# Kernel optimization log

Measured on AMD Instinct MI355X. Metric: run time of the kernel, lower is better.

The kernel has to match this reference:

```python
import jax, jax.numpy as jnp
import numpy as np

N, E, D, L = 100000, 400000, 300, 5
BN_EPS = 1e-5


def setup_inputs() -> dict:
    key = jax.random.key(0)
    ks = jax.random.split(key, 8)
    x = jax.random.randint(ks[0], (N, 7), 0, 5)
    edge_index = jax.random.randint(ks[1], (2, E), 0, N)
    edge_attr = jax.random.randint(ks[2], (E, 4), 0, 2)
    s = 0.1
    atom_tables = jax.random.normal(ks[3], (7, 119, D), jnp.float32) * s
    bond_tables = jax.random.normal(ks[4], (L, 4, 6, D), jnp.float32) * s
    mlp_w1 = jax.random.normal(ks[5], (L, D, 2 * D), jnp.float32) * (1.0 / np.sqrt(D))
    mlp_b1 = jnp.zeros((L, 2 * D), jnp.float32)
    mlp_w2 = jax.random.normal(ks[6], (L, 2 * D, D), jnp.float32) * (1.0 / np.sqrt(2 * D))
    mlp_b2 = jnp.zeros((L, D), jnp.float32)
    bn_gamma = jnp.ones((L, D), jnp.float32)
    bn_beta = jnp.zeros((L, D), jnp.float32)
    return dict(x=x, edge_index=edge_index, edge_attr=edge_attr,
                atom_tables=atom_tables, bond_tables=bond_tables,
                mlp_w1=mlp_w1, mlp_b1=mlp_b1, mlp_w2=mlp_w2, mlp_b2=mlp_b2,
                bn_gamma=bn_gamma, bn_beta=bn_beta)


def reference(x, edge_index, edge_attr, atom_tables, bond_tables,
              mlp_w1, mlp_b1, mlp_w2, mlp_b2, bn_gamma, bn_beta):
    n = x.shape[0]
    # add self loops (PyG add_self_loops appends them)
    loop = jnp.arange(n)
    src = jnp.concatenate([edge_index[0], loop])  # message source j
    dst = jnp.concatenate([edge_index[1], loop])  # aggregation target i
    self_loop_attr = jnp.zeros((n, 4), edge_attr.dtype).at[:, 0].set(4)
    ea = jnp.concatenate([edge_attr, self_loop_attr], axis=0)  # [E+N, 4]

    # AtomEncoder: sum of 7 per-feature embeddings -> [N, D]
    h = atom_tables[jnp.arange(7), x].sum(axis=1)

    for l in range(L):
        # BondEncoder: sum of 4 per-feature embeddings -> [E+N, D]
        e_emb = bond_tables[l][jnp.arange(4), ea].sum(axis=1)
        # GIN message = x_j + edge_emb, aggr='add' by target node
        msg = h[src] + e_emb
        agg = jax.ops.segment_sum(msg, dst, num_segments=n)
        # GIN update MLP: Linear -> ReLU -> Linear
        hid = jax.nn.relu(agg @ mlp_w1[l] + mlp_b1[l])
        out = hid @ mlp_w2[l] + mlp_b2[l]
        # BatchNorm1d (training mode: batch stats, biased var)
        mu = out.mean(axis=0)
        var = out.var(axis=0)
        out = (out - mu) / jnp.sqrt(var + BN_EPS) * bn_gamma[l] + bn_beta[l]
        # drop_ratio = 0.0 -> dropout is identity; ReLU except last layer
        if l < L - 1:
            out = jax.nn.relu(out)
        h = out
    return h  # JK='last'
```

## Files before the change

### kernel.cpp

```cpp
#include <hip/hip_runtime.h>

typedef unsigned short u16;
typedef unsigned int   u32;
typedef __bf16 bf16x8 __attribute__((ext_vector_type(8)));
typedef float  f32x4  __attribute__((ext_vector_type(4)));

__device__ __forceinline__ u16 f2bf(float f) {
    u32 u = __builtin_bit_cast(u32, f);
    u = u + 0x7fffu + ((u >> 16) & 1u);
    return (u16)(u >> 16);
}
__device__ __forceinline__ float bflo(u32 u) { return __builtin_bit_cast(float, u << 16); }
__device__ __forceinline__ float bfhi(u32 u) { return __builtin_bit_cast(float, u & 0xffff0000u); }
__device__ __forceinline__ u32 pack2(float x, float y) { return (u32)f2bf(x) | ((u32)f2bf(y) << 16); }

__device__ __forceinline__ void gll16(const u16* g, u16* l) {
    __builtin_amdgcn_global_load_lds(
        (const __attribute__((address_space(1))) void*)g,
        (__attribute__((address_space(3))) void*)l, 16, 0, 0);
}

#define NN 100000
#define EE 400000
#define DP 320
#define HP 640

__global__ void count_deg(const int* __restrict__ ei, int* __restrict__ deg, int E) {
    int e = blockIdx.x * 256 + threadIdx.x;
    if (e < E) atomicAdd(&deg[ei[E + e]], 1);
}

__global__ void scan1(const int* __restrict__ deg, int* __restrict__ out, int* __restrict__ bsums, int n) {
    __shared__ int lds[1024];
    int t = threadIdx.x;
    int i = blockIdx.x * 1024 + t;
    int v = (i < n) ? deg[i] : 0;
    lds[t] = v;
    __syncthreads();
    for (int d = 1; d < 1024; d <<= 1) {
        int add = (t >= d) ? lds[t - d] : 0;
        __syncthreads();
        lds[t] += add;
        __syncthreads();
    }
    if (i < n) out[i] = lds[t] - v;
    if (t == 1023) bsums[blockIdx.x] = lds[t];
}

__global__ void scan2(int* __restrict__ bsums, int nb) {
    __shared__ int lds[128];
    int t = threadIdx.x;
    int v = (t < nb) ? bsums[t] : 0;
    lds[t] = v;
    __syncthreads();
    for (int d = 1; d < 128; d <<= 1) {
        int add = (t >= d) ? lds[t - d] : 0;
        __syncthreads();
        lds[t] += add;
        __syncthreads();
    }
    if (t < nb) bsums[t] = lds[t] - v;
}

__global__ void scan3(int* __restrict__ out, const int* __restrict__ bsums, int n, int etot) {
    int i = blockIdx.x * 1024 + threadIdx.x;
    if (i < n) out[i] += bsums[blockIdx.x];
    else if (i == n) out[i] = etot;
}

__global__ void fill_csr(const int* __restrict__ ei, const int* __restrict__ ea,
                         int* __restrict__ cursors, u32* __restrict__ vals, int E) {
    int e = blockIdx.x * 256 + threadIdx.x;
    if (e >= E) return;
    int dst = ei[E + e];
    int src = ei[e];
    u32 code = (u32)((ea[e*4] & 1) | ((ea[e*4+1] & 1) << 1) | ((ea[e*4+2] & 1) << 2) | ((ea[e*4+3] & 1) << 3));
    int pos = atomicAdd(&cursors[dst], 1);
    vals[pos] = ((u32)src << 4) | code;
}

__global__ void conv_w1(const float* __restrict__ w, u16* __restrict__ wt) {
    int id = blockIdx.x * 256 + threadIdx.x;
    if (id >= 5 * HP * DP) return;
    int l = id / (HP * DP);
    int rem = id - l * (HP * DP);
    int n = rem / DP;
    int kidx = rem - n * DP;
    int u = kidx >> 3, e = kidx & 7;
    int kk = ((u ^ (n & 7)) << 3) | e;
    u16 v = 0;
    if (n < 600 && kk < 300) v = f2bf(w[((size_t)l * 300 + kk) * 600 + n]);
    wt[id] = v;
}
__global__ void conv_w2(const float* __restrict__ w, u16* __restrict__ wt) {
    int id = blockIdx.x * 256 + threadIdx.x;
    if (id >= 5 * DP * HP) return;
    int l = id / (DP * HP);
    int rem = id - l * (DP * HP);
    int n = rem / HP;
    int kp = rem - n * HP;
    int up = kp >> 3, e = kp & 7;
    int ul = (up & ~3) | ((up & 3) ^ ((n >> 1) & 3));
    int kk = (ul << 3) | e;
    u16 v = 0;
    if (n < 300 && kk < 600) v = f2bf(w[((size_t)l * 600 + kk) * 300 + n]);
    wt[id] = v;
}

__global__ void atom_enc(const int* __restrict__ x, const float* __restrict__ at, u16* __restrict__ y) {
    const int i = blockIdx.x;
    const int d = threadIdx.x;
    __shared__ int xi[7];
    if (d < 7) xi[d] = x[i * 7 + d];
    __syncthreads();
    u16 v = 0;
    if (d < 300) {
        float s = 0.f;
        #pragma unroll
        for (int f = 0; f < 7; ++f) s += at[(f * 119 + xi[f]) * 300 + d];
        v = f2bf(s);
    }
    y[(size_t)i * DP + d] = v;
}

__global__ void bond_enc(const float* __restrict__ bt, float* __restrict__ emb) {
    const int c = blockIdx.x;
    const int d = threadIdx.x;
    float s = 0.f;
    if (d < 300) {
        if (c < 16) {
            #pragma unroll
            for (int f = 0; f < 4; ++f) s += bt[(f * 6 + ((c >> f) & 1)) * 300 + d];
        } else {
            s = bt[4 * 300 + d];
            #pragma unroll
            for (int f = 1; f < 4; ++f) s += bt[f * 6 * 300 + d];
        }
    }
    emb[c * DP + d] = s;
}

__global__ void bn_ss(const float* __restrict__ stats, const float* __restrict__ gamma,
                      const float* __restrict__ beta, float* __restrict__ scale,
                      float* __restrict__ shift, int n) {
    int d = threadIdx.x;
    float sc = 0.f, sh = 0.f;
    if (d < 300) {
        float inv_n = 1.0f / (float)n;
        float mu = stats[d] * inv_n;
        float var = stats[DP + d] * inv_n - mu * mu;
        float inv = 1.0f / sqrtf(var + 1e-5f);
        sc = gamma[d] * inv;
        sh = beta[d] - mu * sc;
    }
    scale[d] = sc; shift[d] = sh;
}

__global__ void bn_apply(const float* __restrict__ hraw, const float* __restrict__ scale,
                         const float* __restrict__ shift, u16* __restrict__ y) {
    const int i = blockIdx.x;
    const int d = threadIdx.x;
    float v = fmaf(scale[d], hraw[(size_t)i * DP + d], shift[d]);
    y[(size_t)i * DP + d] = f2bf(fmaxf(v, 0.f));
}

__global__ void aggregate(const u16* __restrict__ y,
                          const float* __restrict__ emb,
                          const int* __restrict__ offs, const u32* __restrict__ vals,
                          u16* __restrict__ agg, const int n) {
    const int wid = (int)((blockIdx.x * (size_t)blockDim.x + threadIdx.x) >> 6);
    const int lane = threadIdx.x & 63;
    if (wid >= n) return;
    const int j0 = lane, j1 = lane + 64, j2 = lane + 128;
    const bool has2 = (lane < 32);

    float a0x = 0.f, a0y = 0.f, a1x = 0.f, a1y = 0.f, a2x = 0.f, a2y = 0.f;

    auto accum = [&](int srcrow, const float* erow) {
        const u32* row = (const u32*)y + (size_t)srcrow * (DP / 2);
        u32 u0 = row[j0], u1 = row[j1];
        u32 u2 = has2 ? row[j2] : 0u;
        float2 e0 = *(const float2*)(erow + 2 * j0);
        float2 e1 = *(const float2*)(erow + 2 * j1);
        a0x += bflo(u0) + e0.x;  a0y += bfhi(u0) + e0.y;
        a1x += bflo(u1) + e1.x;  a1y += bfhi(u1) + e1.y;
        if (has2) {
            float2 e2 = *(const float2*)(erow + 2 * j2);
            a2x += bflo(u2) + e2.x;  a2y += bfhi(u2) + e2.y;
        }
    };

    accum(wid, emb + 16 * DP);
    const int s = offs[wid], t = offs[wid + 1];
    for (int e = s; e < t; ++e) {
        u32 v = vals[e];
        accum((int)(v >> 4), emb + (v & 15u) * DP);
    }

    u32* out = (u32*)agg + (size_t)wid * (DP / 2);
    out[j0] = pack2(a0x, a0y);
    out[j1] = pack2(a1x, a1y);
    if (has2) out[j2] = pack2(a2x, a2y);
}

__global__ __launch_bounds__(512, 2) void fused_mlp(
    const u16* __restrict__ A,
    const u16* __restrict__ W1t,
    const u16* __restrict__ W2t,
    const float* __restrict__ b1g,
    const float* __restrict__ b2g,
    float* __restrict__ H,
    float* __restrict__ st1, float* __restrict__ st2,
    const int M) {

    __shared__ __align__(16) u16 W1s[2 * 32 * 320];
    __shared__ __align__(16) u16 W2s[2 * 320 * 32];
    __shared__ __align__(16) float hidF[128 * 36];

    const int tid  = threadIdx.x;
    const int bm   = blockIdx.x * 128;
    const int wave = tid >> 6;
    const int lane = tid & 63;
    const int mg   = wave >> 1;
    const int ng   = wave & 1;
    const int l15  = lane & 15;
    const int q    = lane >> 4;

    for (int i = wave; i < 20; i += 8)
        gll16(W1t + (size_t)(i * 64 + lane) * 8, &W1s[i * 512]);
    {
        const u16* g2 = W2t;
        for (int i = wave; i < 20; i += 8) {
            int u = i * 64 + lane;
            gll16(g2 + (size_t)(u >> 2) * HP + (u & 3) * 8, &W2s[i * 512]);
        }
    }

    bf16x8 afr[2][10];
    #pragma unroll
    for (int mf = 0; mf < 2; ++mf) {
        int arow = bm + mg * 32 + mf * 16 + l15;
        if (arow > M - 1) arow = M - 1;
        const u16* ap = A + (size_t)arow * DP + q * 8;
        #pragma unroll
        for (int kt = 0; kt < 10; ++kt)
            afr[mf][kt] = __builtin_bit_cast(bf16x8, *(const uint4*)(ap + kt * 32));
    }

    f32x4 acc2[2][10];
    const f32x4 zero4 = {0.f, 0.f, 0.f, 0.f};
    #pragma unroll
    for (int mf = 0; mf < 2; ++mf)
        #pragma unroll
        for (int nf = 0; nf < 10; ++nf) acc2[mf][nf] = zero4;

    __syncthreads();

    const int rr    = ng * 16 + l15;
    const int rbase = rr * 320;
    const int r7    = l15 & 7;
    const int s2    = (l15 >> 1) & 3;

    for (int c = 0; c < 20; ++c) {
        const int p = c & 1;
        const u16* w1cur = W1s + p * 10240;
        const u16* w2cur = W2s + p * 10240;

        if (c < 19) {
            const u16* g1 = W1t + (size_t)(c + 1) * 10240;
            u16* l1 = W1s + (p ^ 1) * 10240;
            for (int i = wave; i < 20; i += 8)
                gll16(g1 + (size_t)(i * 64 + lane) * 8, l1 + i * 512);
            const u16* g2 = W2t + (size_t)(c + 1) * 32;
            u16* l2 = W2s + (p ^ 1) * 10240;
            for (int i = wave; i < 20; i += 8) {
                int u = i * 64 + lane;
                gll16(g2 + (size_t)(u >> 2) * HP + (u & 3) * 8, l2 + i * 512);
            }
        }

        f32x4 acc1[2] = {zero4, zero4};
        #pragma unroll
        for (int kt = 0; kt < 10; ++kt) {
            uint4 t = *(const uint4*)&w1cur[rbase + ((((kt * 4 + q)) ^ r7) << 3)];
            bf16x8 b = __builtin_bit_cast(bf16x8, t);
            acc1[0] = __builtin_amdgcn_mfma_f32_16x16x32_bf16(afr[0][kt], b, acc1[0], 0, 0, 0);
            acc1[1] = __builtin_amdgcn_mfma_f32_16x16x32_bf16(afr[1][kt], b, acc1[1], 0, 0, 0);
        }
        {
            int gcol = c * 32 + ng * 16 + l15;
            float bb = (gcol < 600) ? b1g[gcol] : 0.f;
            #pragma unroll
            for (int mf = 0; mf < 2; ++mf)
                #pragma unroll
                for (int r = 0; r < 4; ++r)
                    hidF[(mg * 32 + mf * 16 + q * 4 + r) * 36 + ng * 16 + l15] =
                        fmaxf(acc1[mf][r] + bb, 0.f);
        }
        asm volatile("s_waitcnt lgkmcnt(0)" ::: "memory");
        __builtin_amdgcn_s_barrier();
        __builtin_amdgcn_sched_barrier(0);

        bf16x8 a2[2];
        #pragma unroll
        for (int mf = 0; mf < 2; ++mf) {
            const float* hp = &hidF[(mg * 32 + mf * 16 + l15) * 36 + q * 8];
            f32x4 lo = *(const f32x4*)hp;
            f32x4 hi = *(const f32x4*)(hp + 4);
            uint4 w;
            w.x = pack2(lo[0], lo[1]);
            w.y = pack2(lo[2], lo[3]);
            w.z = pack2(hi[0], hi[1]);
            w.w = pack2(hi[2], hi[3]);
            a2[mf] = __builtin_bit_cast(bf16x8, w);
        }
        #pragma unroll
        for (int nf = 0; nf < 10; ++nf) {
            int row = ng * 160 + nf * 16 + l15;
            uint4 t = *(const uint4*)&w2cur[row * 32 + ((q ^ s2) << 3)];
            bf16x8 b = __builtin_bit_cast(bf16x8, t);
            acc2[0][nf] = __builtin_amdgcn_mfma_f32_16x16x32_bf16(a2[0], b, acc2[0][nf], 0, 0, 0);
            acc2[1][nf] = __builtin_amdgcn_mfma_f32_16x16x32_bf16(a2[1], b, acc2[1][nf], 0, 0, 0);
        }
        __syncthreads();
    }

    #pragma unroll
    for (int nf = 0; nf < 10; ++nf) {
        const int col = ng * 160 + nf * 16 + l15;
        const float bb = (col < 300) ? b2g[col] : 0.f;
        float s1 = 0.f, s2v = 0.f;
        #pragma unroll
        for (int mf = 0; mf < 2; ++mf)
            #pragma unroll
            for (int r = 0; r < 4; ++r) {
                const int row = bm + mg * 32 + mf * 16 + q * 4 + r;
                if (row < M) {
                    float v = acc2[mf][nf][r] + bb;
                    H[(size_t)row * DP + col] = v;
                    s1 += v; s2v += v * v;
                }
            }
        s1 += __shfl_xor(s1, 16); s1 += __shfl_xor(s1, 32);
        s2v += __shfl_xor(s2v, 16); s2v += __shfl_xor(s2v, 32);
        if (q == 0) { atomicAdd(&st1[col], s1); atomicAdd(&st2[col], s2v); }
    }
}

__global__ void finalize(const float* __restrict__ hraw, const float* __restrict__ scale,
                         const float* __restrict__ shift, float* __restrict__ out) {
    const int i = blockIdx.x;
    const int d = threadIdx.x;
    if (d < 300) {
        float x = hraw[(size_t)i * DP + d];
        out[(size_t)i * 300 + d] = fmaf(scale[d], x, shift[d]);
    }
}

extern "C" void kernel_launch(void* const* d_in, const int* in_sizes, int n_in,
                              void* d_out, int out_size, void* d_ws, size_t ws_size,
                              hipStream_t stream) {
    const int N = NN, E = EE, L = 5;
    const int*   x     = (const int*)d_in[0];
    const int*   ei    = (const int*)d_in[1];
    const int*   ea    = (const int*)d_in[2];
    const float* at    = (const float*)d_in[3];
    const float* bt    = (const float*)d_in[4];
    const float* w1    = (const float*)d_in[5];
    const float* b1    = (const float*)d_in[6];
    const float* w2    = (const float*)d_in[7];
    const float* b2    = (const float*)d_in[8];
    const float* gamma = (const float*)d_in[9];
    const float* beta  = (const float*)d_in[10];
    float* out = (float*)d_out;

    char* ws = (char*)d_ws;
    size_t off = 0;
    auto alloc = [&](size_t bytes) { char* p = ws + off; off = (off + bytes + 255) & ~(size_t)255; return p; };
    u16* buf_y    = (u16*)alloc((size_t)N * DP * 2);
    u16* buf_agg  = (u16*)alloc((size_t)N * DP * 2);
    float* buf_h  = (float*)alloc((size_t)N * DP * 4);
    u16* w1t      = (u16*)alloc((size_t)5 * HP * DP * 2);
    u16* w2t      = (u16*)alloc((size_t)5 * DP * HP * 2);
    int* deg      = (int*)alloc((size_t)N * 4);
    int* offs     = (int*)alloc((size_t)(N + 1) * 4);
    int* cursors  = (int*)alloc((size_t)N * 4);
    u32* vals     = (u32*)alloc((size_t)E * 4);
    int* bsums    = (int*)alloc(128 * 4);
    float* emb    = (float*)alloc(17 * DP * 4);
    float* stats  = (float*)alloc(2 * DP * 4);
    float* scale  = (float*)alloc(DP * 4);
    float* shift  = (float*)alloc(DP * 4);

    (void)hipMemsetAsync(deg, 0, (size_t)N * 4, stream);
    count_deg<<<(E + 255) / 256, 256, 0, stream>>>(ei, deg, E);
    const int nb = (N + 1023) / 1024;
    scan1<<<nb, 1024, 0, stream>>>(deg, offs, bsums, N);
    scan2<<<1, 128, 0, stream>>>(bsums, nb);
    scan3<<<(N + 1 + 1023) / 1024, 1024, 0, stream>>>(offs, bsums, N, E);
    (void)hipMemcpyAsync(cursors, offs, (size_t)N * 4, hipMemcpyDeviceToDevice, stream);
    fill_csr<<<(E + 255) / 256, 256, 0, stream>>>(ei, ea, cursors, vals, E);

    conv_w1<<<(5 * HP * DP + 255) / 256, 256, 0, stream>>>(w1, w1t);
    conv_w2<<<(5 * DP * HP + 255) / 256, 256, 0, stream>>>(w2, w2t);

    atom_enc<<<N, DP, 0, stream>>>(x, at, buf_y);

    const int MB = (N + 127) / 128;
    for (int l = 0; l < L; ++l) {
        bond_enc<<<17, DP, 0, stream>>>(bt + (size_t)l * 4 * 6 * 300, emb);
        aggregate<<<(N * 64 + 255) / 256, 256, 0, stream>>>(
            buf_y, emb, offs, vals, buf_agg, N);
        (void)hipMemsetAsync(stats, 0, 2 * DP * 4, stream);
        fused_mlp<<<MB, 512, 0, stream>>>(
            buf_agg,
            w1t + (size_t)l * HP * DP, w2t + (size_t)l * DP * HP,
            b1 + (size_t)l * 600, b2 + (size_t)l * 300,
            buf_h, stats, stats + DP, N);
        bn_ss<<<1, DP, 0, stream>>>(stats, gamma + (size_t)l * 300, beta + (size_t)l * 300, scale, shift, N);
        if (l < L - 1)
            bn_apply<<<N, DP, 0, stream>>>(buf_h, scale, shift, buf_y);
    }
    finalize<<<N, DP, 0, stream>>>(buf_h, scale, shift, out);
}
```

Measured before the change: 2.270 ms.

## Widen fused MLP hidden chunks to 64 with single-buffered staged weight loads

The fused MLP kernel now walks the hidden dimension in 10 chunks of 64 instead of 20 chunks of 32. W1 and W2 tiles are single-buffered, and each is refilled right after the barrier that ends its use, so the load overlaps the other GEMM phase. The W2 transpose swizzle is rewritten for 64-wide rows, and s_setprio hints wrap the MFMA loops. This halves the number of chunk iterations and barriers and gives each phase more MFMA work, but it leaves less time to hide each weight load.

```diff
diff --git a/kernel.cpp b/kernel.cpp
--- a/kernel.cpp
+++ b/kernel.cpp
@@ -99,9 +99,10 @@
     int rem = id - l * (DP * HP);
     int n = rem / HP;
     int kp = rem - n * HP;
-    int up = kp >> 3, e = kp & 7;
-    int ul = (up & ~3) | ((up & 3) ^ ((n >> 1) & 3));
-    int kk = (ul << 3) | e;
+    int c = kp >> 6;
+    int j = (kp >> 3) & 7;
+    int e = kp & 7;
+    int kk = c * 64 + ((j ^ (n & 7)) << 3) + e;
     u16 v = 0;
     if (n < 300 && kk < 600) v = f2bf(w[((size_t)l * 600 + kk) * 300 + n]);
     wt[id] = v;
@@ -213,9 +214,9 @@
     float* __restrict__ st1, float* __restrict__ st2,
     const int M) {
 
-    __shared__ __align__(16) u16 W1s[2 * 32 * 320];
-    __shared__ __align__(16) u16 W2s[2 * 320 * 32];
-    __shared__ __align__(16) float hidF[128 * 36];
+    __shared__ __align__(16) u16 W1s[64 * 320];
+    __shared__ __align__(16) u16 W2s[320 * 64];
+    __shared__ __align__(16) float hidF[128 * 68];
 
     const int tid  = threadIdx.x;
     const int bm   = blockIdx.x * 128;
@@ -225,15 +226,18 @@
     const int ng   = wave & 1;
     const int l15  = lane & 15;
     const int q    = lane >> 4;
-
-    for (int i = wave; i < 20; i += 8)
+    const int r7   = l15 & 7;
+
+    #pragma unroll
+    for (int it = 0; it < 5; ++it) {
+        int i = wave + it * 8;
         gll16(W1t + (size_t)(i * 64 + lane) * 8, &W1s[i * 512]);
-    {
-        const u16* g2 = W2t;
-        for (int i = wave; i < 20; i += 8) {
-            int u = i * 64 + lane;
-            gll16(g2 + (size_t)(u >> 2) * HP + (u & 3) * 8, &W2s[i * 512]);
-        }
+    }
+    #pragma unroll
+    for (int it = 0; it < 5; ++it) {
+        int i = wave + it * 8;
+        int u = i * 64 + lane;
+        gll16(W2t + (size_t)(u >> 3) * HP + (u & 7) * 8, &W2s[i * 512]);
     }
 
     bf16x8 afr[2][10];
@@ -256,73 +260,82 @@
 
     __syncthreads();
 
-    const int rr    = ng * 16 + l15;
-    const int rbase = rr * 320;
-    const int r7    = l15 & 7;
-    const int s2    = (l15 >> 1) & 3;
-
-    for (int c = 0; c < 20; ++c) {
-        const int p = c & 1;
-        const u16* w1cur = W1s + p * 10240;
-        const u16* w2cur = W2s + p * 10240;
-
-        if (c < 19) {
-            const u16* g1 = W1t + (size_t)(c + 1) * 10240;
-            u16* l1 = W1s + (p ^ 1) * 10240;
-            for (int i = wave; i < 20; i += 8)
-                gll16(g1 + (size_t)(i * 64 + lane) * 8, l1 + i * 512);
-            const u16* g2 = W2t + (size_t)(c + 1) * 32;
-            u16* l2 = W2s + (p ^ 1) * 10240;
-            for (int i = wave; i < 20; i += 8) {
-                int u = i * 64 + lane;
-                gll16(g2 + (size_t)(u >> 2) * HP + (u & 3) * 8, l2 + i * 512);
-            }
-        }
-
-        f32x4 acc1[2] = {zero4, zero4};
-        #pragma unroll
-        for (int kt = 0; kt < 10; ++kt) {
-            uint4 t = *(const uint4*)&w1cur[rbase + ((((kt * 4 + q)) ^ r7) << 3)];
-            bf16x8 b = __builtin_bit_cast(bf16x8, t);
-            acc1[0] = __builtin_amdgcn_mfma_f32_16x16x32_bf16(afr[0][kt], b, acc1[0], 0, 0, 0);
-            acc1[1] = __builtin_amdgcn_mfma_f32_16x16x32_bf16(afr[1][kt], b, acc1[1], 0, 0, 0);
-        }
-        {
-            int gcol = c * 32 + ng * 16 + l15;
+    for (int c = 0; c < 10; ++c) {
+        f32x4 acc1[2][2] = {{zero4, zero4}, {zero4, zero4}};
+        __builtin_amdgcn_s_setprio(1);
+        #pragma unroll
+        for (int sc = 0; sc < 2; ++sc) {
+            const int rb = (sc * 32 + ng * 16 + l15) * 320;
+            #pragma unroll
+            for (int kt = 0; kt < 10; ++kt) {
+                uint4 t = *(const uint4*)&W1s[rb + (((kt * 4 + q) ^ r7) << 3)];
+                bf16x8 b = __builtin_bit_cast(bf16x8, t);
+                acc1[sc][0] = __builtin_amdgcn_mfma_f32_16x16x32_bf16(afr[0][kt], b, acc1[sc][0], 0, 0, 0);
+                acc1[sc][1] = __builtin_amdgcn_mfma_f32_16x16x32_bf16(afr[1][kt], b, acc1[sc][1], 0, 0, 0);
+            }
+        }
+        __builtin_amdgcn_s_setprio(0);
+        #pragma unroll
+        for (int sc = 0; sc < 2; ++sc) {
+            int gcol = c * 64 + sc * 32 + ng * 16 + l15;
             float bb = (gcol < 600) ? b1g[gcol] : 0.f;
             #pragma unroll
             for (int mf = 0; mf < 2; ++mf)
                 #pragma unroll
                 for (int r = 0; r < 4; ++r)
-                    hidF[(mg * 32 + mf * 16 + q * 4 + r) * 36 + ng * 16 + l15] =
-                        fmaxf(acc1[mf][r] + bb, 0.f);
-        }
-        asm volatile("s_waitcnt lgkmcnt(0)" ::: "memory");
-        __builtin_amdgcn_s_barrier();
-        __builtin_amdgcn_sched_barrier(0);
-
-        bf16x8 a2[2];
-        #pragma unroll
-        for (int mf = 0; mf < 2; ++mf) {
-            const float* hp = &hidF[(mg * 32 + mf * 16 + l15) * 36 + q * 8];
-            f32x4 lo = *(const f32x4*)hp;
-            f32x4 hi = *(const f32x4*)(hp + 4);
-            uint4 w;
-            w.x = pack2(lo[0], lo[1]);
-            w.y = pack2(lo[2], lo[3]);
-            w.z = pack2(hi[0], hi[1]);
-            w.w = pack2(hi[2], hi[3]);
-            a2[mf] = __builtin_bit_cast(bf16x8, w);
-        }
+                    hidF[(mg * 32 + mf * 16 + q * 4 + r) * 68 + sc * 32 + ng * 16 + l15] =
+                        fmaxf(acc1[sc][mf][r] + bb, 0.f);
+        }
+        __syncthreads();
+
+        if (c < 9) {
+            const u16* g1 = W1t + (size_t)(c + 1) * 20480;
+            #pragma unroll
+            for (int it = 0; it < 5; ++it) {
+                int i = wave + it * 8;
+                gll16(g1 + (size_t)(i * 64 + lane) * 8, &W1s[i * 512]);
+            }
+        }
+
+        bf16x8 a2[2][2];
+        #pragma unroll
+        for (int mf = 0; mf < 2; ++mf)
+            #pragma unroll
+            for (int kq = 0; kq < 2; ++kq) {
+                const float* hp = &hidF[(mg * 32 + mf * 16 + l15) * 68 + kq * 32 + q * 8];
+                f32x4 lo = *(const f32x4*)hp;
+                f32x4 hi = *(const f32x4*)(hp + 4);
+                uint4 w;
+                w.x = pack2(lo[0], lo[1]);
+                w.y = pack2(lo[2], lo[3]);
+                w.z = pack2(hi[0], hi[1]);
+                w.w = pack2(hi[2], hi[3]);
+                a2[mf][kq] = __builtin_bit_cast(bf16x8, w);
+            }
+        __builtin_amdgcn_s_setprio(1);
         #pragma unroll
         for (int nf = 0; nf < 10; ++nf) {
-            int row = ng * 160 + nf * 16 + l15;
-            uint4 t = *(const uint4*)&w2cur[row * 32 + ((q ^ s2) << 3)];
-            bf16x8 b = __builtin_bit_cast(bf16x8, t);
-            acc2[0][nf] = __builtin_amdgcn_mfma_f32_16x16x32_bf16(a2[0], b, acc2[0][nf], 0, 0, 0);
-            acc2[1][nf] = __builtin_amdgcn_mfma_f32_16x16x32_bf16(a2[1], b, acc2[1][nf], 0, 0, 0);
-        }
-        __syncthreads();
+            const int row = ng * 160 + nf * 16 + l15;
+            #pragma unroll
+            for (int kq = 0; kq < 2; ++kq) {
+                uint4 t = *(const uint4*)&W2s[row * 64 + (((kq * 4 + q) ^ r7) << 3)];
+                bf16x8 b = __builtin_bit_cast(bf16x8, t);
+                acc2[0][nf] = __builtin_amdgcn_mfma_f32_16x16x32_bf16(a2[0][kq], b, acc2[0][nf], 0, 0, 0);
+                acc2[1][nf] = __builtin_amdgcn_mfma_f32_16x16x32_bf16(a2[1][kq], b, acc2[1][nf], 0, 0, 0);
+            }
+        }
+        __builtin_amdgcn_s_setprio(0);
+        __syncthreads();
+
+        if (c < 9) {
+            const u16* g2 = W2t + (size_t)(c + 1) * 64;
+            #pragma unroll
+            for (int it = 0; it < 5; ++it) {
+                int i = wave + it * 8;
+                int u = i * 64 + lane;
+                gll16(g2 + (size_t)(u >> 3) * HP + (u & 7) * 8, &W2s[i * 512]);
+            }
+        }
     }
 
     #pragma unroll
```

After: 1.993 ms. 12.2% less time.

## Shrink fused MLP tile to 64 rows, single-buffer weights with split prefetch

Applied to the files above, without the earlier changes.

Halves the fused MLP block to 64 rows and 256 threads and replaces the double-buffered W1/W2 LDS staging with single buffers. The next chunk's W1 is now loaded after the first GEMM and the next W2 after the second GEMM, each behind a barrier. s_setprio is raised around the MFMA loops. The aim is to cut LDS use so more blocks fit per CU and raise occupancy. The cost is that weights get reloaded per smaller tile, doubling total weight traffic, and the loads overlap less with compute.

```diff
diff --git a/kernel.cpp b/kernel.cpp
--- a/kernel.cpp
+++ b/kernel.cpp
@@ -203,7 +203,7 @@
     if (has2) out[j2] = pack2(a2x, a2y);
 }
 
-__global__ __launch_bounds__(512, 2) void fused_mlp(
+__global__ __launch_bounds__(256, 2) void fused_mlp(
     const u16* __restrict__ A,
     const u16* __restrict__ W1t,
     const u16* __restrict__ W2t,
@@ -213,27 +213,31 @@
     float* __restrict__ st1, float* __restrict__ st2,
     const int M) {
 
-    __shared__ __align__(16) u16 W1s[2 * 32 * 320];
-    __shared__ __align__(16) u16 W2s[2 * 320 * 32];
-    __shared__ __align__(16) float hidF[128 * 36];
+    __shared__ __align__(16) u16 W1s[32 * 320];
+    __shared__ __align__(16) u16 W2s[320 * 32];
+    __shared__ __align__(16) float hidF[64 * 36];
 
     const int tid  = threadIdx.x;
-    const int bm   = blockIdx.x * 128;
+    const int bm   = blockIdx.x * 64;
     const int wave = tid >> 6;
     const int lane = tid & 63;
     const int mg   = wave >> 1;
     const int ng   = wave & 1;
     const int l15  = lane & 15;
     const int q    = lane >> 4;
-
-    for (int i = wave; i < 20; i += 8)
+    const int r7   = l15 & 7;
+    const int s2   = (l15 >> 1) & 3;
+
+    #pragma unroll
+    for (int it = 0; it < 5; ++it) {
+        int i = wave + it * 4;
         gll16(W1t + (size_t)(i * 64 + lane) * 8, &W1s[i * 512]);
-    {
-        const u16* g2 = W2t;
-        for (int i = wave; i < 20; i += 8) {
-            int u = i * 64 + lane;
-            gll16(g2 + (size_t)(u >> 2) * HP + (u & 3) * 8, &W2s[i * 512]);
-        }
+    }
+    #pragma unroll
+    for (int it = 0; it < 5; ++it) {
+        int i = wave + it * 4;
+        int u = i * 64 + lane;
+        gll16(W2t + (size_t)(u >> 2) * HP + (u & 3) * 8, &W2s[i * 512]);
     }
 
     bf16x8 afr[2][10];
@@ -256,37 +260,19 @@
 
     __syncthreads();
 
-    const int rr    = ng * 16 + l15;
-    const int rbase = rr * 320;
-    const int r7    = l15 & 7;
-    const int s2    = (l15 >> 1) & 3;
+    const int rb = (ng * 16 + l15) * 320;
 
     for (int c = 0; c < 20; ++c) {
-        const int p = c & 1;
-        const u16* w1cur = W1s + p * 10240;
-        const u16* w2cur = W2s + p * 10240;
-
-        if (c < 19) {
-            const u16* g1 = W1t + (size_t)(c + 1) * 10240;
-            u16* l1 = W1s + (p ^ 1) * 10240;
-            for (int i = wave; i < 20; i += 8)
-                gll16(g1 + (size_t)(i * 64 + lane) * 8, l1 + i * 512);
-            const u16* g2 = W2t + (size_t)(c + 1) * 32;
-            u16* l2 = W2s + (p ^ 1) * 10240;
-            for (int i = wave; i < 20; i += 8) {
-                int u = i * 64 + lane;
-                gll16(g2 + (size_t)(u >> 2) * HP + (u & 3) * 8, l2 + i * 512);
-            }
-        }
-
         f32x4 acc1[2] = {zero4, zero4};
+        __builtin_amdgcn_s_setprio(1);
         #pragma unroll
         for (int kt = 0; kt < 10; ++kt) {
-            uint4 t = *(const uint4*)&w1cur[rbase + ((((kt * 4 + q)) ^ r7) << 3)];
+            uint4 t = *(const uint4*)&W1s[rb + (((kt * 4 + q) ^ r7) << 3)];
             bf16x8 b = __builtin_bit_cast(bf16x8, t);
             acc1[0] = __builtin_amdgcn_mfma_f32_16x16x32_bf16(afr[0][kt], b, acc1[0], 0, 0, 0);
             acc1[1] = __builtin_amdgcn_mfma_f32_16x16x32_bf16(afr[1][kt], b, acc1[1], 0, 0, 0);
         }
+        __builtin_amdgcn_s_setprio(0);
         {
             int gcol = c * 32 + ng * 16 + l15;
             float bb = (gcol < 600) ? b1g[gcol] : 0.f;
@@ -297,9 +283,16 @@
                     hidF[(mg * 32 + mf * 16 + q * 4 + r) * 36 + ng * 16 + l15] =
                         fmaxf(acc1[mf][r] + bb, 0.f);
         }
-        asm volatile("s_waitcnt lgkmcnt(0)" ::: "memory");
-        __builtin_amdgcn_s_barrier();
-        __builtin_amdgcn_sched_barrier(0);
+        __syncthreads();
+
+        if (c < 19) {
+            const u16* g1 = W1t + (size_t)(c + 1) * 10240;
+            #pragma unroll
+            for (int it = 0; it < 5; ++it) {
+                int i = wave + it * 4;
+                gll16(g1 + (size_t)(i * 64 + lane) * 8, &W1s[i * 512]);
+            }
+        }
 
         bf16x8 a2[2];
         #pragma unroll
@@ -314,15 +307,27 @@
             w.w = pack2(hi[2], hi[3]);
             a2[mf] = __builtin_bit_cast(bf16x8, w);
         }
+        __builtin_amdgcn_s_setprio(1);
         #pragma unroll
         for (int nf = 0; nf < 10; ++nf) {
             int row = ng * 160 + nf * 16 + l15;
-            uint4 t = *(const uint4*)&w2cur[row * 32 + ((q ^ s2) << 3)];
+            uint4 t = *(const uint4*)&W2s[row * 32 + ((q ^ s2) << 3)];
             bf16x8 b = __builtin_bit_cast(bf16x8, t);
             acc2[0][nf] = __builtin_amdgcn_mfma_f32_16x16x32_bf16(a2[0], b, acc2[0][nf], 0, 0, 0);
             acc2[1][nf] = __builtin_amdgcn_mfma_f32_16x16x32_bf16(a2[1], b, acc2[1][nf], 0, 0, 0);
         }
-        __syncthreads();
+        __builtin_amdgcn_s_setprio(0);
+        __syncthreads();
+
+        if (c < 19) {
+            const u16* g2 = W2t + (size_t)(c + 1) * 32;
+            #pragma unroll
+            for (int it = 0; it < 5; ++it) {
+                int i = wave + it * 4;
+                int u = i * 64 + lane;
+                gll16(g2 + (size_t)(u >> 2) * HP + (u & 3) * 8, &W2s[i * 512]);
+            }
+        }
     }
 
     #pragma unroll
@@ -406,13 +411,13 @@
 
     atom_enc<<<N, DP, 0, stream>>>(x, at, buf_y);
 
-    const int MB = (N + 127) / 128;
+    const int MB = (N + 63) / 64;
     for (int l = 0; l < L; ++l) {
         bond_enc<<<17, DP, 0, stream>>>(bt + (size_t)l * 4 * 6 * 300, emb);
         aggregate<<<(N * 64 + 255) / 256, 256, 0, stream>>>(
             buf_y, emb, offs, vals, buf_agg, N);
         (void)hipMemsetAsync(stats, 0, 2 * DP * 4, stream);
-        fused_mlp<<<MB, 512, 0, stream>>>(
+        fused_mlp<<<MB, 256, 0, stream>>>(
             buf_agg,
             w1t + (size_t)l * HP * DP, w2t + (size_t)l * DP * HP,
             b1 + (size_t)l * 600, b2 + (size_t)l * 300,
```

After: 2.046 ms. 1.11x faster.

## Software-pipeline the fused MLP's two GEMMs and vectorize aggregate row loads

Applied to the files above, without the earlier changes.

In the fused MLP kernel, the hidden buffer is now double-buffered. The second GEMM for chunk c-1 is issued in the same iteration as the first GEMM for chunk c, so each iteration needs one barrier instead of two. W2 chunks are now loaded one iteration ahead of use, and s_setprio raises priority around the MFMA section. The aggregate kernel now has 40 lanes each load 8 bf16 values with one 16-byte access instead of three 4-byte loads per lane. The cost is more LDS for the second hidden buffer and somewhat more register pressure.

```diff
diff --git a/kernel.cpp b/kernel.cpp
--- a/kernel.cpp
+++ b/kernel.cpp
@@ -171,22 +171,21 @@
     const int wid = (int)((blockIdx.x * (size_t)blockDim.x + threadIdx.x) >> 6);
     const int lane = threadIdx.x & 63;
     if (wid >= n) return;
-    const int j0 = lane, j1 = lane + 64, j2 = lane + 128;
-    const bool has2 = (lane < 32);
-
-    float a0x = 0.f, a0y = 0.f, a1x = 0.f, a1y = 0.f, a2x = 0.f, a2y = 0.f;
+    const bool act = (lane < 40);
+
+    float acc[8];
+    #pragma unroll
+    for (int i = 0; i < 8; ++i) acc[i] = 0.f;
 
     auto accum = [&](int srcrow, const float* erow) {
-        const u32* row = (const u32*)y + (size_t)srcrow * (DP / 2);
-        u32 u0 = row[j0], u1 = row[j1];
-        u32 u2 = has2 ? row[j2] : 0u;
-        float2 e0 = *(const float2*)(erow + 2 * j0);
-        float2 e1 = *(const float2*)(erow + 2 * j1);
-        a0x += bflo(u0) + e0.x;  a0y += bfhi(u0) + e0.y;
-        a1x += bflo(u1) + e1.x;  a1y += bfhi(u1) + e1.y;
-        if (has2) {
-            float2 e2 = *(const float2*)(erow + 2 * j2);
-            a2x += bflo(u2) + e2.x;  a2y += bfhi(u2) + e2.y;
+        if (act) {
+            uint4 v = *(const uint4*)(y + (size_t)srcrow * DP + lane * 8);
+            float4 e0 = *(const float4*)(erow + lane * 8);
+            float4 e1 = *(const float4*)(erow + lane * 8 + 4);
+            acc[0] += bflo(v.x) + e0.x;  acc[1] += bfhi(v.x) + e0.y;
+            acc[2] += bflo(v.y) + e0.z;  acc[3] += bfhi(v.y) + e0.w;
+            acc[4] += bflo(v.z) + e1.x;  acc[5] += bfhi(v.z) + e1.y;
+            acc[6] += bflo(v.w) + e1.z;  acc[7] += bfhi(v.w) + e1.w;
         }
     };
 
@@ -197,10 +196,14 @@
         accum((int)(v >> 4), emb + (v & 15u) * DP);
     }
 
-    u32* out = (u32*)agg + (size_t)wid * (DP / 2);
-    out[j0] = pack2(a0x, a0y);
-    out[j1] = pack2(a1x, a1y);
-    if (has2) out[j2] = pack2(a2x, a2y);
+    if (act) {
+        uint4 o;
+        o.x = pack2(acc[0], acc[1]);
+        o.y = pack2(acc[2], acc[3]);
+        o.z = pack2(acc[4], acc[5]);
+        o.w = pack2(acc[6], acc[7]);
+        *(uint4*)(agg + (size_t)wid * DP + lane * 8) = o;
+    }
 }
 
 __global__ __launch_bounds__(512, 2) void fused_mlp(
@@ -213,9 +216,9 @@
     float* __restrict__ st1, float* __restrict__ st2,
     const int M) {
 
-    __shared__ __align__(16) u16 W1s[2 * 32 * 320];
-    __shared__ __align__(16) u16 W2s[2 * 320 * 32];
-    __shared__ __align__(16) float hidF[128 * 36];
+    __shared__ __align__(16) u16 W1s[2][32 * 320];
+    __shared__ __align__(16) u16 W2s[2][320 * 32];
+    __shared__ __align__(16) float hidF[2][128 * 36];
 
     const int tid  = threadIdx.x;
     const int bm   = blockIdx.x * 128;
@@ -225,16 +228,11 @@
     const int ng   = wave & 1;
     const int l15  = lane & 15;
     const int q    = lane >> 4;
+    const int r7   = l15 & 7;
+    const int s2   = (l15 >> 1) & 3;
 
     for (int i = wave; i < 20; i += 8)
-        gll16(W1t + (size_t)(i * 64 + lane) * 8, &W1s[i * 512]);
-    {
-        const u16* g2 = W2t;
-        for (int i = wave; i < 20; i += 8) {
-            int u = i * 64 + lane;
-            gll16(g2 + (size_t)(u >> 2) * HP + (u & 3) * 8, &W2s[i * 512]);
-        }
-    }
+        gll16(W1t + (size_t)(i * 64 + lane) * 8, &W1s[0][i * 512]);
 
     bf16x8 afr[2][10];
     #pragma unroll
@@ -256,37 +254,58 @@
 
     __syncthreads();
 
-    const int rr    = ng * 16 + l15;
-    const int rbase = rr * 320;
-    const int r7    = l15 & 7;
-    const int s2    = (l15 >> 1) & 3;
+    const int rb = (ng * 16 + l15) * 320;
 
     for (int c = 0; c < 20; ++c) {
-        const int p = c & 1;
-        const u16* w1cur = W1s + p * 10240;
-        const u16* w2cur = W2s + p * 10240;
+        const int pc = c & 1;
 
         if (c < 19) {
             const u16* g1 = W1t + (size_t)(c + 1) * 10240;
-            u16* l1 = W1s + (p ^ 1) * 10240;
             for (int i = wave; i < 20; i += 8)
-                gll16(g1 + (size_t)(i * 64 + lane) * 8, l1 + i * 512);
-            const u16* g2 = W2t + (size_t)(c + 1) * 32;
-            u16* l2 = W2s + (p ^ 1) * 10240;
+                gll16(g1 + (size_t)(i * 64 + lane) * 8, &W1s[pc ^ 1][i * 512]);
+        }
+        {
+            const u16* g2 = W2t + (size_t)c * 32;
             for (int i = wave; i < 20; i += 8) {
                 int u = i * 64 + lane;
-                gll16(g2 + (size_t)(u >> 2) * HP + (u & 3) * 8, l2 + i * 512);
+                gll16(g2 + (size_t)(u >> 2) * HP + (u & 3) * 8, &W2s[pc][i * 512]);
             }
         }
 
+        __builtin_amdgcn_s_setprio(1);
+        if (c > 0) {
+            bf16x8 a2[2];
+            #pragma unroll
+            for (int mf = 0; mf < 2; ++mf) {
+                const float* hp = &hidF[pc ^ 1][(mg * 32 + mf * 16 + l15) * 36 + q * 8];
+                f32x4 lo = *(const f32x4*)hp;
+                f32x4 hi = *(const f32x4*)(hp + 4);
+                uint4 w;
+                w.x = pack2(lo[0], lo[1]);
+                w.y = pack2(lo[2], lo[3]);
+                w.z = pack2(hi[0], hi[1]);
+                w.w = pack2(hi[2], hi[3]);
+                a2[mf] = __builtin_bit_cast(bf16x8, w);
+            }
+            #pragma unroll
+            for (int nf = 0; nf < 10; ++nf) {
+                int row = ng * 160 + nf * 16 + l15;
+                uint4 t = *(const uint4*)&W2s[pc ^ 1][row * 32 + ((q ^ s2) << 3)];
+                bf16x8 b = __builtin_bit_cast(bf16x8, t);
+                acc2[0][nf] = __builtin_amdgcn_mfma_f32_16x16x32_bf16(a2[0], b, acc2[0][nf], 0, 0, 0);
+                acc2[1][nf] = __builtin_amdgcn_mfma_f32_16x16x32_bf16(a2[1], b, acc2[1][nf], 0, 0, 0);
+            }
+        }
+
         f32x4 acc1[2] = {zero4, zero4};
         #pragma unroll
         for (int kt = 0; kt < 10; ++kt) {
-            uint4 t = *(const uint4*)&w1cur[rbase + ((((kt * 4 + q)) ^ r7) << 3)];
+            uint4 t = *(const uint4*)&W1s[pc][rb + (((kt * 4 + q) ^ r7) << 3)];
             bf16x8 b = __builtin_bit_cast(bf16x8, t);
             acc1[0] = __builtin_amdgcn_mfma_f32_16x16x32_bf16(afr[0][kt], b, acc1[0], 0, 0, 0);
             acc1[1] = __builtin_amdgcn_mfma_f32_16x16x32_bf16(afr[1][kt], b, acc1[1], 0, 0, 0);
         }
+        __builtin_amdgcn_s_setprio(0);
         {
             int gcol = c * 32 + ng * 16 + l15;
             float bb = (gcol < 600) ? b1g[gcol] : 0.f;
@@ -294,17 +313,17 @@
             for (int mf = 0; mf < 2; ++mf)
                 #pragma unroll
                 for (int r = 0; r < 4; ++r)
-                    hidF[(mg * 32 + mf * 16 + q * 4 + r) * 36 + ng * 16 + l15] =
+                    hidF[pc][(mg * 32 + mf * 16 + q * 4 + r) * 36 + ng * 16 + l15] =
                         fmaxf(acc1[mf][r] + bb, 0.f);
         }
-        asm volatile("s_waitcnt lgkmcnt(0)" ::: "memory");
-        __builtin_amdgcn_s_barrier();
-        __builtin_amdgcn_sched_barrier(0);
-
+        __syncthreads();
+    }
+
+    {
         bf16x8 a2[2];
         #pragma unroll
         for (int mf = 0; mf < 2; ++mf) {
-            const float* hp = &hidF[(mg * 32 + mf * 16 + l15) * 36 + q * 8];
+            const float* hp = &hidF[1][(mg * 32 + mf * 16 + l15) * 36 + q * 8];
             f32x4 lo = *(const f32x4*)hp;
             f32x4 hi = *(const f32x4*)(hp + 4);
             uint4 w;
@@ -317,12 +336,11 @@
         #pragma unroll
         for (int nf = 0; nf < 10; ++nf) {
             int row = ng * 160 + nf * 16 + l15;
-            uint4 t = *(const uint4*)&w2cur[row * 32 + ((q ^ s2) << 3)];
+            uint4 t = *(const uint4*)&W2s[1][row * 32 + ((q ^ s2) << 3)];
             bf16x8 b = __builtin_bit_cast(bf16x8, t);
             acc2[0][nf] = __builtin_amdgcn_mfma_f32_16x16x32_bf16(a2[0], b, acc2[0][nf], 0, 0, 0);
             acc2[1][nf] = __builtin_amdgcn_mfma_f32_16x16x32_bf16(a2[1], b, acc2[1][nf], 0, 0, 0);
         }
-        __syncthreads();
     }
 
     #pragma unroll
```

Result: faster. 2.153 ms (-5.2%).
